# Performance work log

Hardware: AMD Instinct MI355X
Metric: run time of the kernel (lower is better)

Reference implementation:

```python
import jax, jax.numpy as jnp
import numpy as np

QMIN, QMAX = 0, 255        # 8-bit asymmetric activation quant bounds
GROUP_SIZE = 128

def setup_inputs() -> dict:
    key = jax.random.key(0)
    k1, k2, k3, k4, k5 = jax.random.split(key, 5)
    x = jax.random.normal(k1, (1, 2048, 4096), dtype=jnp.float32)
    qweight = jax.random.randint(k2, (4096, 32, 128), 0, 16, dtype=jnp.int32)  # uint4 codes
    w_scales = jax.random.uniform(k3, (4096, 32), dtype=jnp.float32, minval=0.001, maxval=0.02)
    w_zero_points = jax.random.randint(k4, (4096, 32), 0, 16, dtype=jnp.int32)
    bias = jax.random.normal(k5, (4096,), dtype=jnp.float32)
    return {"x": x, "qweight": qweight, "w_scales": w_scales,
            "w_zero_points": w_zero_points, "bias": bias}

def reference(x, qweight, w_scales, w_zero_points, bias):
    xf = x.astype(jnp.float32)
    # per-token (last-dim) asymmetric dynamic activation quantization
    xmin = jnp.min(xf, axis=-1, keepdims=True)
    xmax = jnp.max(xf, axis=-1, keepdims=True)
    x_scale = jnp.clip((xmax - xmin) / (QMAX - QMIN), 1e-5, None)
    x_zp = jnp.clip(jnp.round(-xmin / x_scale), QMIN, QMAX)
    q = jnp.clip(jnp.round(xf / x_scale) + x_zp, QMIN, QMAX)
    centered_x = (q - x_zp).reshape(*x.shape[:-1], -1, GROUP_SIZE)  # [B,S,G,C]
    # grouped weight dequant (zero-point centered)
    centered_w = qweight.astype(jnp.float32) - w_zero_points.astype(jnp.float32)[..., None]  # [O,G,C]
    acc = jnp.einsum('bsgc,ogc->bsog', centered_x, centered_w)  # [B,S,O,G]
    out = (acc * w_scales[None, None]).sum(axis=-1)  # apply per-group weight scales
    out = out * x_scale  # per-token activation scale
    out = out + bias
    return out
```

## Files before the change

kernel.cpp:

```cpp
#include <hip/hip_runtime.h>
#include <stdint.h>

#define M_DIM 2048
#define N_DIM 4096
#define K_DIM 4096
#define NGROUP 32
#define GSIZE 128

#define RQ_UP   (127.0f / 15.0f)
#define RQ_DOWN (15.0f / 127.0f)

#define BM 128
#define BN 128
#define KSLICE 64
#define NSLICE (K_DIM / KSLICE)
#define ASLOT (BM * KSLICE)
#define BSLOT (BN * KSLICE)

typedef __attribute__((ext_vector_type(4))) int int32x4_t;

static __device__ __forceinline__ void gl2lds16(const void* g, void* l) {
    auto gp = (const __attribute__((address_space(1))) unsigned int*)(uintptr_t)g;
    auto lp = (__attribute__((address_space(3))) unsigned int*)(uintptr_t)l;
    __builtin_amdgcn_global_load_lds(gp, lp, 16, 0, 0);
}

#define WAITVM_(N) asm volatile("s_waitcnt vmcnt(" #N ")")
#define WAITVM(N)                                   \
    do {                                            \
        __builtin_amdgcn_sched_barrier(0);          \
        WAITVM_(N);                                 \
        __builtin_amdgcn_sched_barrier(0);          \
    } while (0)

#define QUANT_BLOCKS M_DIM
#define DEQ_BLOCKS ((N_DIM * K_DIM) / 8 / 256)

__global__ __launch_bounds__(256) void prep_kernel(
        const float* __restrict__ x,
        const int* __restrict__ qw,
        const float* __restrict__ wsc,
        const int* __restrict__ wzp,
        char* __restrict__ A8,
        char* __restrict__ Bt8,
        float* __restrict__ xscale,
        float* __restrict__ xzpc,
        int* __restrict__ Sw)
{
    const int t = threadIdx.x;
    if (blockIdx.x < QUANT_BLOCKS) {
        const int s = blockIdx.x;
        const float* xrow = x + (size_t)s * K_DIM;

        float xv[16];
        float vmin = 1e38f, vmax = -1e38f;
#pragma unroll
        for (int p = 0; p < 4; ++p) {
            float4 v = *((const float4*)(xrow + p * 1024) + t);
            xv[p*4+0] = v.x; xv[p*4+1] = v.y; xv[p*4+2] = v.z; xv[p*4+3] = v.w;
            vmin = fminf(vmin, fminf(fminf(v.x, v.y), fminf(v.z, v.w)));
            vmax = fmaxf(vmax, fmaxf(fmaxf(v.x, v.y), fmaxf(v.z, v.w)));
        }
#pragma unroll
        for (int off = 32; off > 0; off >>= 1) {
            vmin = fminf(vmin, __shfl_xor(vmin, off));
            vmax = fmaxf(vmax, __shfl_xor(vmax, off));
        }
        __shared__ float smin[4], smax[4];
        const int wave = t >> 6;
        if ((t & 63) == 0) { smin[wave] = vmin; smax[wave] = vmax; }
        __syncthreads();
        vmin = fminf(fminf(smin[0], smin[1]), fminf(smin[2], smin[3]));
        vmax = fmaxf(fmaxf(smax[0], smax[1]), fmaxf(smax[2], smax[3]));

        float sc = (vmax - vmin) / 255.0f;
        sc = fmaxf(sc, 1e-5f);
        float zp = rintf(-vmin / sc);
        zp = fminf(fmaxf(zp, 0.0f), 255.0f);
        const float inv_sc = 1.0f / sc;

#pragma unroll
        for (int p = 0; p < 4; ++p) {
            int b[4];
#pragma unroll
            for (int e = 0; e < 4; ++e) {
                float q = fminf(fmaxf(rintf(xv[p*4+e] * inv_sc) + zp, 0.0f), 255.0f);
                b[e] = (int)q - 128;
            }
            unsigned pack = (b[0] & 0xff) | ((b[1] & 0xff) << 8) |
                            ((b[2] & 0xff) << 16) | ((b[3] & 0xff) << 24);
            *(unsigned*)(A8 + (size_t)s * K_DIM + p * 1024 + t * 4) = pack;
        }
        if (t == 0) { xscale[s] = sc; xzpc[s] = 128.0f - zp; }
    } else {
        const size_t base = ((size_t)(blockIdx.x - QUANT_BLOCKS) * 256 + t) * 8;
        const int n = (int)(base >> 12);
        const int g = (int)((base >> 7) & 31);
        const int zp = wzp[n * NGROUP + g];

        const int cl = t & 15;
        float2 wp = *(const float2*)(wsc + (size_t)n * NGROUP + cl * 2);
        float smx = fmaxf(wp.x, wp.y);
#pragma unroll
        for (int off = 1; off < 16; off <<= 1)
            smx = fmaxf(smx, __shfl_xor(smx, off));
        const float factor = wsc[n * NGROUP + g] * (RQ_UP / smx);

        int4 c0 = *(const int4*)(qw + base);
        int4 c1 = *(const int4*)(qw + base + 4);
        int w[8];
        w[0] = (int)rintf((float)(c0.x - zp) * factor);
        w[1] = (int)rintf((float)(c0.y - zp) * factor);
        w[2] = (int)rintf((float)(c0.z - zp) * factor);
        w[3] = (int)rintf((float)(c0.w - zp) * factor);
        w[4] = (int)rintf((float)(c1.x - zp) * factor);
        w[5] = (int)rintf((float)(c1.y - zp) * factor);
        w[6] = (int)rintf((float)(c1.z - zp) * factor);
        w[7] = (int)rintf((float)(c1.w - zp) * factor);
        uint2 pk;
        pk.x = (w[0] & 0xff) | ((w[1] & 0xff) << 8) | ((w[2] & 0xff) << 16) | ((w[3] & 0xff) << 24);
        pk.y = (w[4] & 0xff) | ((w[5] & 0xff) << 8) | ((w[6] & 0xff) << 16) | ((w[7] & 0xff) << 24);
        *(uint2*)(Bt8 + base) = pk;

        int s8 = w[0] + w[1] + w[2] + w[3] + w[4] + w[5] + w[6] + w[7];
#pragma unroll
        for (int off = 1; off < 16; off <<= 1) s8 += __shfl_xor(s8, off);
        if ((t & 15) == 0)
            Sw[n * NGROUP + g] = s8;
    }
}

__global__ __launch_bounds__(256, 2) void gemm_kernel(
        const char* __restrict__ A8,
        const char* __restrict__ Bt8,
        const float* __restrict__ xscale,
        const float* __restrict__ xzpc,
        const float* __restrict__ wsc,
        const int* __restrict__ Sw,
        const float* __restrict__ bias,
        float* __restrict__ out)
{
    __shared__ __align__(16) char As[4][ASLOT];
    __shared__ __align__(16) char Bs[4][BSLOT];
    __shared__ float fws_s[BN], wsf_s[BN];

    const int tid  = threadIdx.x;
    const int bn   = blockIdx.x;
    const int bm   = blockIdx.y;
    const int wave = tid >> 6;
    const int lane = tid & 63;
    const int wr   = wave >> 1;
    const int wcl  = wave & 1;
    const int lrow  = lane & 15;
    const int lquad = lane >> 4;

    if (tid < BN) {
        const int n = bn * BN + tid;
        const int4* s4 = (const int4*)(Sw + (size_t)n * NGROUP);
        int acc = 0;
#pragma unroll
        for (int p = 0; p < 8; ++p) { int4 v = s4[p]; acc += v.x + v.y + v.z + v.w; }
        const float4* w4 = (const float4*)(wsc + (size_t)n * NGROUP);
        float s = 0.f;
#pragma unroll
        for (int p = 0; p < 8; ++p) {
            float4 w = w4[p];
            s = fmaxf(s, fmaxf(fmaxf(w.x, w.y), fmaxf(w.z, w.w)));
        }
        const float fw = s * RQ_DOWN;
        fws_s[tid] = fw;
        wsf_s[tid] = fw * (float)acc;
    }
    __builtin_amdgcn_sched_barrier(0);
    asm volatile("s_waitcnt vmcnt(0) lgkmcnt(0)");
    __builtin_amdgcn_sched_barrier(0);

    const char* Ab = A8  + (size_t)(bm * BM) * K_DIM;
    const char* Bb = Bt8 + (size_t)(bn * BN) * K_DIM;
    const int lsub = lane >> 2;
    const int csrc = (lane & 3) ^ ((lane >> 3) & 3);
    const char* gA0 = Ab + (size_t)((wave * 16     ) + lsub) * K_DIM + csrc * 16;
    const char* gA1 = Ab + (size_t)((wave * 16 + 64) + lsub) * K_DIM + csrc * 16;
    const char* gB0 = Bb + (size_t)((wave * 16     ) + lsub) * K_DIM + csrc * 16;
    const char* gB1 = Bb + (size_t)((wave * 16 + 64) + lsub) * K_DIM + csrc * 16;
    const int lOF = wave * 1024;

    const int xq = (lquad ^ ((lrow >> 1) & 3)) * 16;
    const unsigned asBase = (unsigned)(uintptr_t)&As[0][0];
    const unsigned bsBase = (unsigned)(uintptr_t)&Bs[0][0];
    const unsigned aOff0 = (unsigned)((wr  * 64 + lrow) * KSLICE + xq);
    const unsigned bOff0 = (unsigned)((wcl * 64 + lrow) * KSLICE + xq);

    int32x4_t iacc[4][4];
    const int32x4_t zi = {0, 0, 0, 0};
#pragma unroll
    for (int i = 0; i < 4; ++i)
#pragma unroll
        for (int j = 0; j < 4; ++j) iacc[i][j] = zi;

#define STAGE(t) {                                                    \
        const int sl_ = (t) & 3;                                      \
        const size_t k0_ = (size_t)(t) * KSLICE;                      \
        gl2lds16(gA0 + k0_, &As[sl_][0] + lOF);                       \
        gl2lds16(gA1 + k0_, &As[sl_][0] + 4096 + lOF);                \
        gl2lds16(gB0 + k0_, &Bs[sl_][0] + lOF);                       \
        gl2lds16(gB1 + k0_, &Bs[sl_][0] + 4096 + lOF);                \
    }

#define READ8(aAdr, bAdr, a0, a1, a2, a3, b0, b1, b2, b3)             \
    asm volatile(                                                     \
        "ds_read_b128 %0, %8 offset:0\n\t"                            \
        "ds_read_b128 %1, %8 offset:1024\n\t"                         \
        "ds_read_b128 %2, %8 offset:2048\n\t"                         \
        "ds_read_b128 %3, %8 offset:3072\n\t"                         \
        "ds_read_b128 %4, %9 offset:0\n\t"                            \
        "ds_read_b128 %5, %9 offset:1024\n\t"                         \
        "ds_read_b128 %6, %9 offset:2048\n\t"                         \
        "ds_read_b128 %7, %9 offset:3072\n\t"                         \
        "s_waitcnt lgkmcnt(0)"                                        \
        : "=&v"(a0), "=&v"(a1), "=&v"(a2), "=&v"(a3),                 \
          "=&v"(b0), "=&v"(b1), "=&v"(b2), "=&v"(b3)                  \
        : "v"(aAdr), "v"(bAdr))

#define MFMAS(a0, a1, a2, a3, b0, b1, b2, b3) {                       \
        int32x4_t av_[4] = {a0, a1, a2, a3};                          \
        int32x4_t bv_[4] = {b0, b1, b2, b3};                          \
        __builtin_amdgcn_s_setprio(1);                                \
        _Pragma("unroll")                                             \
        for (int i_ = 0; i_ < 4; ++i_)                                \
            _Pragma("unroll")                                         \
            for (int j_ = 0; j_ < 4; ++j_)                            \
                iacc[i_][j_] = __builtin_amdgcn_mfma_i32_16x16x64_i8( \
                    av_[i_], bv_[j_], iacc[i_][j_], 0, 0, 0);         \
        __builtin_amdgcn_s_setprio(0);                                \
    }

#define BODY(s, VMN, DOSTAGE) {                                       \
        if (DOSTAGE) STAGE((s) + 3);                                  \
        WAITVM(VMN);                                                  \
        __builtin_amdgcn_s_barrier();                                 \
        const unsigned sl_ = (unsigned)((s) & 3) * 8192u;             \
        int32x4_t a0_, a1_, a2_, a3_, b0_, b1_, b2_, b3_;             \
        READ8(asBase + sl_ + aOff0, bsBase + sl_ + bOff0,             \
              a0_, a1_, a2_, a3_, b0_, b1_, b2_, b3_);                \
        MFMAS(a0_, a1_, a2_, a3_, b0_, b1_, b2_, b3_);                \
        __builtin_amdgcn_s_barrier();                                 \
    }

    STAGE(0); STAGE(1); STAGE(2);

    for (int s = 0; s <= NSLICE - 4; ++s)
        BODY(s, 12, 1);
    BODY(NSLICE - 3, 8, 0);
    BODY(NSLICE - 2, 4, 0);
    BODY(NSLICE - 1, 0, 0);

    float fn[4], wf[4], bb[4];
    int ncol[4];
#pragma unroll
    for (int j = 0; j < 4; ++j) {
        const int ncl = wcl * 64 + j * 16 + lrow;
        ncol[j] = bn * BN + ncl;
        fn[j] = fws_s[ncl];
        wf[j] = wsf_s[ncl];
        bb[j] = bias[ncol[j]];
    }
    const int m0 = bm * BM + wr * 64;
#pragma unroll
    for (int i = 0; i < 4; ++i) {
#pragma unroll
        for (int r = 0; r < 4; ++r) {
            const int m = m0 + i * 16 + lquad * 4 + r;
            const float xs  = xscale[m];
            const float czp = xzpc[m];
            float* orow = out + (size_t)m * N_DIM;
#pragma unroll
            for (int j = 0; j < 4; ++j)
                orow[ncol[j]] = xs * (fn[j] * (float)iacc[i][j][r] + czp * wf[j]) + bb[j];
        }
    }
#undef BODY
#undef MFMAS
#undef READ8
#undef STAGE
}

extern "C" void kernel_launch(void* const* d_in, const int* in_sizes, int n_in,
                              void* d_out, int out_size, void* d_ws, size_t ws_size,
                              hipStream_t stream) {
    const float* x     = (const float*)d_in[0];
    const int*   qw    = (const int*)d_in[1];
    const float* wsc   = (const float*)d_in[2];
    const int*   wzp   = (const int*)d_in[3];
    const float* bias  = (const float*)d_in[4];
    float* out = (float*)d_out;

    char* A8  = (char*)d_ws;
    char* Bt8 = A8 + (size_t)M_DIM * K_DIM;
    float* xscale = (float*)(Bt8 + (size_t)N_DIM * K_DIM);
    float* xzpc   = xscale + M_DIM;
    int*   Sw     = (int*)(xzpc + M_DIM);

    prep_kernel<<<QUANT_BLOCKS + DEQ_BLOCKS, 256, 0, stream>>>(
        x, qw, wsc, wzp, A8, Bt8, xscale, xzpc, Sw);
    dim3 grid(N_DIM / BN, M_DIM / BM);
    gemm_kernel<<<grid, 256, 0, stream>>>(A8, Bt8, xscale, xzpc, wsc, Sw, bias, out);
}
```

Baseline: 176.2 us.

## Software-pipeline LDS fragment reads one slice ahead of MFMAs with register double-buffering

Restructures the GEMM main loop so each iteration issues ds_read_b128 loads for the next K-slice into a second register set, then runs the MFMAs on the current slice's registers. The blocking lgkmcnt(0) wait is replaced with a partial lgkmcnt(8) wait, which lets LDS read latency overlap with matrix-core work. The vmcnt thresholds and the prologue/epilogue are adjusted to keep the 4-slot global-to-LDS ring consistent. The cost is doubled fragment registers, which may lower occupancy, plus more complex stage accounting.

```diff
diff --git a/kernel.cpp b/kernel.cpp
--- a/kernel.cpp
+++ b/kernel.cpp
@@ -30,6 +30,19 @@
     do {                                            \
         __builtin_amdgcn_sched_barrier(0);          \
         WAITVM_(N);                                 \
+        __builtin_amdgcn_sched_barrier(0);          \
+    } while (0)
+#define WAITLGKM_(N) asm volatile("s_waitcnt lgkmcnt(" #N ")")
+#define WAITLGKM(N)                                 \
+    do {                                            \
+        __builtin_amdgcn_sched_barrier(0);          \
+        WAITLGKM_(N);                               \
+        __builtin_amdgcn_sched_barrier(0);          \
+    } while (0)
+#define BARRIER()                                   \
+    do {                                            \
+        __builtin_amdgcn_sched_barrier(0);          \
+        __builtin_amdgcn_s_barrier();               \
         __builtin_amdgcn_sched_barrier(0);          \
     } while (0)
 
@@ -216,8 +229,7 @@
         "ds_read_b128 %4, %9 offset:0\n\t"                            \
         "ds_read_b128 %5, %9 offset:1024\n\t"                         \
         "ds_read_b128 %6, %9 offset:2048\n\t"                         \
-        "ds_read_b128 %7, %9 offset:3072\n\t"                         \
-        "s_waitcnt lgkmcnt(0)"                                        \
+        "ds_read_b128 %7, %9 offset:3072"                             \
         : "=&v"(a0), "=&v"(a1), "=&v"(a2), "=&v"(a3),                 \
           "=&v"(b0), "=&v"(b1), "=&v"(b2), "=&v"(b3)                  \
         : "v"(aAdr), "v"(bAdr))
@@ -235,25 +247,42 @@
         __builtin_amdgcn_s_setprio(0);                                \
     }
 
-#define BODY(s, VMN, DOSTAGE) {                                       \
+    int32x4_t aA0, aA1, aA2, aA3, bA0, bA1, bA2, bA3;
+    int32x4_t aB0, aB1, aB2, aB3, bB0, bB1, bB2, bB3;
+
+#define BODY(s, VMN, DOSTAGE, CA0,CA1,CA2,CA3,CB0,CB1,CB2,CB3,        \
+             NA0,NA1,NA2,NA3,NB0,NB1,NB2,NB3) {                       \
         if (DOSTAGE) STAGE((s) + 3);                                  \
         WAITVM(VMN);                                                  \
-        __builtin_amdgcn_s_barrier();                                 \
-        const unsigned sl_ = (unsigned)((s) & 3) * 8192u;             \
-        int32x4_t a0_, a1_, a2_, a3_, b0_, b1_, b2_, b3_;             \
+        BARRIER();                                                    \
+        const unsigned sl_ = (unsigned)(((s) + 1) & 3) * 8192u;       \
         READ8(asBase + sl_ + aOff0, bsBase + sl_ + bOff0,             \
-              a0_, a1_, a2_, a3_, b0_, b1_, b2_, b3_);                \
-        MFMAS(a0_, a1_, a2_, a3_, b0_, b1_, b2_, b3_);                \
-        __builtin_amdgcn_s_barrier();                                 \
+              NA0, NA1, NA2, NA3, NB0, NB1, NB2, NB3);                \
+        WAITLGKM(8);                                                  \
+        MFMAS(CA0, CA1, CA2, CA3, CB0, CB1, CB2, CB3);                \
+        BARRIER();                                                    \
     }
 
     STAGE(0); STAGE(1); STAGE(2);
-
-    for (int s = 0; s <= NSLICE - 4; ++s)
-        BODY(s, 12, 1);
-    BODY(NSLICE - 3, 8, 0);
-    BODY(NSLICE - 2, 4, 0);
-    BODY(NSLICE - 1, 0, 0);
+    WAITVM(8);
+    BARRIER();
+    READ8(asBase + aOff0, bsBase + bOff0,
+          aA0, aA1, aA2, aA3, bA0, bA1, bA2, bA3);
+
+    for (int s = 0; s < NSLICE - 4; s += 2) {
+        BODY(s,     8, 1, aA0,aA1,aA2,aA3,bA0,bA1,bA2,bA3,
+                          aB0,aB1,aB2,aB3,bB0,bB1,bB2,bB3);
+        BODY(s + 1, 8, 1, aB0,aB1,aB2,aB3,bB0,bB1,bB2,bB3,
+                          aA0,aA1,aA2,aA3,bA0,bA1,bA2,bA3);
+    }
+    BODY(60, 8, 1, aA0,aA1,aA2,aA3,bA0,bA1,bA2,bA3,
+                   aB0,aB1,aB2,aB3,bB0,bB1,bB2,bB3);
+    BODY(61, 4, 0, aB0,aB1,aB2,aB3,bB0,bB1,bB2,bB3,
+                   aA0,aA1,aA2,aA3,bA0,bA1,bA2,bA3);
+    BODY(62, 0, 0, aA0,aA1,aA2,aA3,bA0,bA1,bA2,bA3,
+                   aB0,aB1,aB2,aB3,bB0,bB1,bB2,bB3);
+    WAITLGKM(0);
+    MFMAS(aB0,aB1,aB2,aB3,bB0,bB1,bB2,bB3);
 
     float fn[4], wf[4], bb[4];
     int ncol[4];
```

Result: faster. 171.1 us (-2.9%).
